# Kernel tuning notes

Hardware: AMD Instinct MI355X
Metric: run time of the kernel (lower is better)

The kernel has to match this reference:

```python
import jax, jax.numpy as jnp
import numpy as np
import math

HIDDEN = 1024
Q_SIZE = 1024
KV_SIZE = 1024
OUT_SIZE = 1024
N_HEADS = 16
D_K = HIDDEN // N_HEADS


def setup_inputs() -> dict:
    key = jax.random.key(0)
    ks = jax.random.split(key, 9)
    b, s, t = 8, 2048, 512
    sc = 0.02
    return {
        "hiddens": jax.random.normal(ks[0], (b, s, KV_SIZE), jnp.float32),
        "query_hiddens": jax.random.normal(ks[1], (b, t, Q_SIZE), jnp.float32),
        "mask": jax.random.randint(ks[2], (b, s), 0, 2, jnp.int32),
        "W_q": jax.random.normal(ks[3], (Q_SIZE, HIDDEN), jnp.float32) * sc,
        "b_q": jnp.zeros((HIDDEN,), jnp.float32),
        "W_k": jax.random.normal(ks[4], (KV_SIZE, HIDDEN), jnp.float32) * sc,
        "W_v": jax.random.normal(ks[5], (KV_SIZE, HIDDEN), jnp.float32) * sc,
        "W_o": jax.random.normal(ks[6], (HIDDEN, OUT_SIZE), jnp.float32) * sc,
        "b_o": jnp.zeros((OUT_SIZE,), jnp.float32),
    }


def reference(hiddens, query_hiddens, mask, W_q, b_q, W_k, W_v, W_o, b_o):
    b, t, _ = query_hiddens.shape
    s = hiddens.shape[1]
    # projections (dropout p=0 in eval -> identity)
    Q = (query_hiddens @ W_q + b_q).reshape(b, t, N_HEADS, D_K)
    K = (hiddens @ W_k).reshape(b, s, N_HEADS, D_K)
    V = (hiddens @ W_v).reshape(b, s, N_HEADS, D_K)
    # scores: [b, t, s, h] matching e = (Q*K).sum(-1)/sqrt(d_k)
    e = jnp.einsum('bthd,bshd->btsh', Q, K) / math.sqrt(D_K)
    neg = (1.0 - mask.astype(e.dtype)) * (-1e20)  # [b, s]
    e = e + neg[:, None, :, None]
    a = jax.nn.softmax(e, axis=2)  # softmax over seqlen
    concat = jnp.einsum('btsh,bshd->bthd', a, V).reshape(b, t, HIDDEN)
    context = concat @ W_o + b_o
    return context, a.mean(axis=-1)
```

## Files before the change

kernel.cpp:

```cpp
#include <hip/hip_runtime.h>
#include <hip/hip_bf16.h>

using short8 = __attribute__((ext_vector_type(8))) short;
using f32x4  = __attribute__((ext_vector_type(4))) float;

#define LSK 72

#define GLDS(gptr, lptr) __builtin_amdgcn_global_load_lds( \
    (const __attribute__((address_space(1))) void*)(gptr), \
    (__attribute__((address_space(3))) void*)(lptr), 16, 0, 0)

static __device__ __forceinline__ short f2b(float f) {
    unsigned u = __builtin_bit_cast(unsigned, f);
    unsigned r = (u + 0x7fffu + ((u >> 16) & 1u)) >> 16;
    return (short)r;
}

__global__ void cvt_bf16(const float* __restrict__ in, short* __restrict__ out, int n) {
    int i = (blockIdx.x * 256 + threadIdx.x) * 4;
    if (i >= n) return;
    float4 v = *(const float4*)(in + i);
    short4 o = make_short4(f2b(v.x), f2b(v.y), f2b(v.z), f2b(v.w));
    *(short4*)(out + i) = o;
}

__global__ void cvt_t_bf16(const float* __restrict__ W, short* __restrict__ Wt, int K, int N) {
    __shared__ short tile[32][33];
    int n0 = blockIdx.x * 32, k0 = blockIdx.y * 32;
    int tx = threadIdx.x, ty = threadIdx.y;
#pragma unroll
    for (int i = 0; i < 4; i++) {
        int r = ty + i * 8;
        tile[r][tx] = f2b(W[(size_t)(k0 + r) * N + n0 + tx]);
    }
    __syncthreads();
#pragma unroll
    for (int i = 0; i < 4; i++) {
        int r = ty + i * 8;
        Wt[(size_t)(n0 + r) * K + k0 + tx] = tile[tx][r];
    }
}

__global__ __launch_bounds__(256) void gemm128(
    const short* __restrict__ A, const short* __restrict__ Bt,
    const float* __restrict__ bias, void* __restrict__ Cout, void* __restrict__ Cout2,
    int M, int mode)
{
    __shared__ short As[128 * 64];
    __shared__ short Bs[128 * 64];
    const int tid = threadIdx.x;
    const int w = tid >> 6, L = tid & 63, quad = L >> 4, l16 = L & 15;

    const int lin = blockIdx.y * gridDim.x + blockIdx.x;
    const int xcd = lin & 7, idx = lin >> 3;
    const int mPer = gridDim.y >> 3;
    const int my = xcd * mPer + idx / gridDim.x;
    const int nx = idx % gridDim.x;
    const int n0 = nx * 128, m0 = my * 128;

    const int K = 1024;
    const int mrow0 = (w >> 1) * 64, ncol0 = (w & 1) * 64;

    const int srow_in = L >> 3;
    const int sgcol   = ((L & 7) ^ (srow_in & 7)) * 8;

    f32x4 acc[4][4];
#pragma unroll
    for (int mi = 0; mi < 4; mi++)
#pragma unroll
        for (int ni = 0; ni < 4; ni++) acc[mi][ni] = (f32x4){0.f, 0.f, 0.f, 0.f};

    for (int k0 = 0; k0 < K; k0 += 64) {
#pragma unroll
        for (int j = 0; j < 4; j++) {
            int c = w * 4 + j;
            int row = c * 8 + srow_in;
            const short* ga = A  + (size_t)(m0 + row) * K + k0 + sgcol;
            const short* gb = Bt + (size_t)(n0 + row) * K + k0 + sgcol;
            GLDS(ga, &As[c * 512]);
            GLDS(gb, &Bs[c * 512]);
        }
        __syncthreads();
#pragma unroll
        for (int kk = 0; kk < 64; kk += 32) {
            int swz = (((kk >> 3) + quad) ^ (l16 & 7)) << 3;
            short8 af[4], bf[4];
#pragma unroll
            for (int mi = 0; mi < 4; mi++)
                af[mi] = *(const short8*)&As[(mrow0 + mi * 16 + l16) * 64 + swz];
#pragma unroll
            for (int ni = 0; ni < 4; ni++)
                bf[ni] = *(const short8*)&Bs[(ncol0 + ni * 16 + l16) * 64 + swz];
#pragma unroll
            for (int mi = 0; mi < 4; mi++)
#pragma unroll
                for (int ni = 0; ni < 4; ni++)
                    acc[mi][ni] = __builtin_amdgcn_mfma_f32_16x16x32_bf16(af[mi], bf[ni], acc[mi][ni], 0, 0, 0);
        }
        __syncthreads();
    }
#pragma unroll
    for (int ni = 0; ni < 4; ni++) {
        int n = n0 + ncol0 + ni * 16 + l16;
        float bv = (mode != 2 && bias) ? bias[n] : 0.f;
#pragma unroll
        for (int mi = 0; mi < 4; mi++) {
#pragma unroll
            for (int r = 0; r < 4; r++) {
                int m = m0 + mrow0 + mi * 16 + quad * 4 + r;
                float v = acc[mi][ni][r] + bv;
                if (mode == 1)      ((float*)Cout)[(size_t)m * 1024 + n] = v;
                else if (mode == 0) ((short*)Cout)[(size_t)m * 1024 + n] = f2b(v);
                else {
                    if (n < 1024) ((short*)Cout)[(size_t)m * 1024 + n] = f2b(v);
                    else {
                        int h = (n - 1024) >> 6, d = n & 63;
                        int b = m >> 11, s = m & 2047;
                        ((short*)Cout2)[(((size_t)b * 16 + h) * 64 + d) * 2048 + s] = f2b(v);
                    }
                }
            }
        }
    }
}

__global__ __launch_bounds__(512) void attn_flash(
    const short* __restrict__ Qb, const short* __restrict__ Kb, const short* __restrict__ Vtb,
    const int* __restrict__ mask, short* __restrict__ Cb, float* __restrict__ lse)
{
    __shared__ short Qs[128 * 64];
    __shared__ short Ks[128 * 64];
    __shared__ short Vts[128 * 64];
    __shared__ short Ps[128 * LSK];
    __shared__ float neg[128];
    const int tid = threadIdx.x;
    const int w = tid >> 6, L = tid & 63, quad = L >> 4, l16 = L & 15;
    const int t0 = blockIdx.x * 128, h = blockIdx.y, b = blockIdx.z;
    const int S = 2048, T = 512, H = 1024;
    const int trow = w * 16;
    const int srow = L >> 3;
    const int sg   = ((L & 7) ^ srow) * 8;

#pragma unroll
    for (int j = 0; j < 2; j++) {
        int row = w * 16 + j * 8 + srow;
        GLDS(Qb + ((size_t)b * T + t0 + row) * H + h * 64 + sg, &Qs[(w * 16 + j * 8) * 64]);
    }
    __syncthreads();
    short8 aq[2];
#pragma unroll
    for (int kk = 0; kk < 2; kk++)
        aq[kk] = *(const short8*)&Qs[(trow + l16) * 64 + ((kk * 4 + quad) ^ (l16 & 7)) * 8];

    f32x4 Oacc[4];
#pragma unroll
    for (int nt = 0; nt < 4; nt++) Oacc[nt] = (f32x4){0.f, 0.f, 0.f, 0.f};
    float lsum[4] = {0.f, 0.f, 0.f, 0.f};

    for (int s0 = 0; s0 < S; s0 += 128) {
#pragma unroll
        for (int j = 0; j < 2; j++) {
            int krow = w * 16 + j * 8 + srow;
            GLDS(Kb + ((size_t)b * S + s0 + krow) * H + h * 64 + sg, &Ks[(w * 16 + j * 8) * 64]);
            int c = w * 2 + j, hf = c >> 3, d0 = (c & 7) * 8;
            GLDS(Vtb + (((size_t)b * 16 + h) * 64 + d0 + srow) * S + s0 + hf * 64 + sg, &Vts[c * 512]);
        }
        if (tid < 128) neg[tid] = mask[(size_t)b * S + s0 + tid] ? 0.f : -1e20f;
        __syncthreads();
#pragma unroll
        for (int hf = 0; hf < 2; hf++) {
            f32x4 sacc[4];
#pragma unroll
            for (int nt = 0; nt < 4; nt++) sacc[nt] = (f32x4){0.f, 0.f, 0.f, 0.f};
#pragma unroll
            for (int kk = 0; kk < 2; kk++) {
#pragma unroll
                for (int nt = 0; nt < 4; nt++) {
                    short8 bf = *(const short8*)&Ks[(hf * 64 + nt * 16 + l16) * 64 + ((kk * 4 + quad) ^ (l16 & 7)) * 8];
                    sacc[nt] = __builtin_amdgcn_mfma_f32_16x16x32_bf16(aq[kk], bf, sacc[nt], 0, 0, 0);
                }
            }
#pragma unroll
            for (int nt = 0; nt < 4; nt++) {
                float ng = neg[hf * 64 + nt * 16 + l16];
#pragma unroll
                for (int r = 0; r < 4; r++) {
                    float e = __expf(fmaf(sacc[nt][r], 0.125f, ng));
                    lsum[r] += e;
                    Ps[(trow + quad * 4 + r) * LSK + nt * 16 + l16] = f2b(e);
                }
            }
#pragma unroll
            for (int kk = 0; kk < 2; kk++) {
                short8 af = *(const short8*)&Ps[(trow + l16) * LSK + kk * 32 + quad * 8];
#pragma unroll
                for (int nt = 0; nt < 4; nt++) {
                    short8 bf = *(const short8*)&Vts[hf * 4096 + (nt * 16 + l16) * 64 + ((kk * 4 + quad) ^ (l16 & 7)) * 8];
                    Oacc[nt] = __builtin_amdgcn_mfma_f32_16x16x32_bf16(af, bf, Oacc[nt], 0, 0, 0);
                }
            }
        }
        __syncthreads();
    }
#pragma unroll
    for (int r = 0; r < 4; r++) {
#pragma unroll
        for (int off = 1; off < 16; off <<= 1)
            lsum[r] += __shfl_xor(lsum[r], off, 64);
    }
#pragma unroll
    for (int r = 0; r < 4; r++) {
        float inv = 1.0f / lsum[r];
        int t = t0 + trow + quad * 4 + r;
#pragma unroll
        for (int nt = 0; nt < 4; nt++) {
            int d = nt * 16 + l16;
            Cb[((size_t)b * T + t) * H + h * 64 + d] = f2b(Oacc[nt][r] * inv);
        }
        if (l16 == 0)
            lse[((size_t)b * 16 + h) * T + t] = __logf(lsum[r]);
    }
}

__global__ __launch_bounds__(256) void attn_amean(
    const short* __restrict__ Qb, const short* __restrict__ Kb,
    const int* __restrict__ mask, const float* __restrict__ lse, float* __restrict__ outA)
{
    __shared__ short Qs[64 * 64];
    __shared__ short Ks[64 * 64];
    __shared__ float neg[64];
    __shared__ float lss[16 * 64];
    const int tid = threadIdx.x;
    const int w = tid >> 6, L = tid & 63, quad = L >> 4, l16 = L & 15;
    const int s0 = blockIdx.x * 64, t0 = blockIdx.y * 64, b = blockIdx.z;
    const int S = 2048, T = 512, H = 1024;
    const int srow = L >> 3;
    const int sg   = ((L & 7) ^ srow) * 8;

    if (tid < 64) neg[tid] = mask[(size_t)b * S + s0 + tid] ? 0.f : -1e20f;
    for (int i = tid; i < 16 * 64; i += 256) {
        int hh = i >> 6, tt = i & 63;
        lss[i] = lse[((size_t)b * 16 + hh) * T + t0 + tt];
    }
    float am[4][4] = {};
    for (int h = 0; h < 16; h++) {
        __syncthreads();
#pragma unroll
        for (int j = 0; j < 2; j++) {
            int row = w * 16 + j * 8 + srow;
            GLDS(Qb + ((size_t)b * T + t0 + row) * H + h * 64 + sg, &Qs[(w * 16 + j * 8) * 64]);
            GLDS(Kb + ((size_t)b * S + s0 + row) * H + h * 64 + sg, &Ks[(w * 16 + j * 8) * 64]);
        }
        __syncthreads();
        short8 aq[2];
#pragma unroll
        for (int kk = 0; kk < 2; kk++)
            aq[kk] = *(const short8*)&Qs[(w * 16 + l16) * 64 + ((kk * 4 + quad) ^ (l16 & 7)) * 8];
        f32x4 sacc[4];
#pragma unroll
        for (int nt = 0; nt < 4; nt++) sacc[nt] = (f32x4){0.f, 0.f, 0.f, 0.f};
#pragma unroll
        for (int kk = 0; kk < 2; kk++) {
#pragma unroll
            for (int nt = 0; nt < 4; nt++) {
                short8 bf = *(const short8*)&Ks[(nt * 16 + l16) * 64 + ((kk * 4 + quad) ^ (l16 & 7)) * 8];
                sacc[nt] = __builtin_amdgcn_mfma_f32_16x16x32_bf16(aq[kk], bf, sacc[nt], 0, 0, 0);
            }
        }
#pragma unroll
        for (int nt = 0; nt < 4; nt++) {
            float ng = neg[nt * 16 + l16];
#pragma unroll
            for (int r = 0; r < 4; r++) {
                int trow = w * 16 + quad * 4 + r;
                am[nt][r] += __expf(fmaf(sacc[nt][r], 0.125f, ng - lss[h * 64 + trow]));
            }
        }
    }
#pragma unroll
    for (int r = 0; r < 4; r++) {
        int t = t0 + w * 16 + quad * 4 + r;
#pragma unroll
        for (int nt = 0; nt < 4; nt++) {
            int s = s0 + nt * 16 + l16;
            outA[((size_t)b * T + t) * S + s] = am[nt][r] * 0.0625f;
        }
    }
}

extern "C" void kernel_launch(void* const* d_in, const int* in_sizes, int n_in,
                              void* d_out, int out_size, void* d_ws, size_t ws_size,
                              hipStream_t stream) {
    const float* hiddens = (const float*)d_in[0];
    const float* query   = (const float*)d_in[1];
    const int*   mask    = (const int*)d_in[2];
    const float* W_q = (const float*)d_in[3];
    const float* b_q = (const float*)d_in[4];
    const float* W_k = (const float*)d_in[5];
    const float* W_v = (const float*)d_in[6];
    const float* W_o = (const float*)d_in[7];
    const float* b_o = (const float*)d_in[8];
    float* out = (float*)d_out;

    constexpr size_t N_H  = 8UL * 2048 * 1024;
    constexpr size_t N_QH = 8UL * 512 * 1024;
    constexpr size_t N_W  = 1024UL * 1024;
    char* ws = (char*)d_ws;
    short* Hb   = (short*)(ws);
    short* QHb  = (short*)(ws + N_H * 2);
    short* Wqt  = (short*)(ws + N_H * 2 + N_QH * 2);
    short* Wkt  = Wqt + N_W;
    short* Wvt  = Wkt + N_W;
    short* Wot  = Wvt + N_W;
    short* Qb   = Wot + N_W;
    short* Kb   = Qb + N_QH;
    short* Vtb  = Kb + N_H;
    short* Cb   = Vtb + N_H;
    float* lseP = (float*)(Cb + N_QH);

    cvt_bf16<<<16384, 256, 0, stream>>>(hiddens, Hb, (int)N_H);
    cvt_bf16<<<4096, 256, 0, stream>>>(query, QHb, (int)N_QH);
    dim3 tgrid(32, 32), tblk(32, 8);
    cvt_t_bf16<<<tgrid, tblk, 0, stream>>>(W_q, Wqt, 1024, 1024);
    cvt_t_bf16<<<tgrid, tblk, 0, stream>>>(W_k, Wkt, 1024, 1024);
    cvt_t_bf16<<<tgrid, tblk, 0, stream>>>(W_v, Wvt, 1024, 1024);
    cvt_t_bf16<<<tgrid, tblk, 0, stream>>>(W_o, Wot, 1024, 1024);

    gemm128<<<dim3(8, 32), 256, 0, stream>>>(QHb, Wqt, b_q, Qb, nullptr, 4096, 0);
    gemm128<<<dim3(16, 128), 256, 0, stream>>>(Hb, Wkt, nullptr, Kb, Vtb, 16384, 2);

    attn_flash<<<dim3(4, 16, 8), 512, 0, stream>>>(Qb, Kb, Vtb, mask, Cb, lseP);

    gemm128<<<dim3(8, 32), 256, 0, stream>>>(Cb, Wot, b_o, out, nullptr, 4096, 1);
    attn_amean<<<dim3(32, 8, 8), 256, 0, stream>>>(Qb, Kb, mask, lseP, out + N_QH);
}
```

Baseline: 433.8 us.

## Shrink GEMM tile to 128x64 and merge weight transpose launches

The GEMM tile moves from 128x128 to 128x64. Each wave now computes 32x64 and the loads are split across waves as 16 A chunks and 8 B chunks, which doubles the grid for the Q, KV and output projections and adds a launch_bounds occupancy hint. The aim is better CU occupancy and load balance on the small 4096-row GEMMs, paid for with lower data reuse per tile and more global traffic for the A operand. The four weight transpose-convert kernels are also merged into one launch using blockIdx.z.

```diff
diff --git a/kernel.cpp b/kernel.cpp
--- a/kernel.cpp
+++ b/kernel.cpp
@@ -24,8 +24,14 @@
     *(short4*)(out + i) = o;
 }
 
-__global__ void cvt_t_bf16(const float* __restrict__ W, short* __restrict__ Wt, int K, int N) {
+__global__ void cvt_t4(const float* __restrict__ W0, const float* __restrict__ W1,
+                       const float* __restrict__ W2, const float* __restrict__ W3,
+                       short* __restrict__ Wt0) {
     __shared__ short tile[32][33];
+    const float* Ws[4] = {W0, W1, W2, W3};
+    const float* W = Ws[blockIdx.z];
+    short* Wt = Wt0 + (size_t)blockIdx.z * 1024 * 1024;
+    const int K = 1024, N = 1024;
     int n0 = blockIdx.x * 32, k0 = blockIdx.y * 32;
     int tx = threadIdx.x, ty = threadIdx.y;
 #pragma unroll
@@ -41,13 +47,13 @@
     }
 }
 
-__global__ __launch_bounds__(256) void gemm128(
+__global__ __launch_bounds__(256, 4) void gemm128(
     const short* __restrict__ A, const short* __restrict__ Bt,
     const float* __restrict__ bias, void* __restrict__ Cout, void* __restrict__ Cout2,
     int M, int mode)
 {
     __shared__ short As[128 * 64];
-    __shared__ short Bs[128 * 64];
+    __shared__ short Bs[64 * 64];
     const int tid = threadIdx.x;
     const int w = tid >> 6, L = tid & 63, quad = L >> 4, l16 = L & 15;
 
@@ -56,43 +62,44 @@
     const int mPer = gridDim.y >> 3;
     const int my = xcd * mPer + idx / gridDim.x;
     const int nx = idx % gridDim.x;
-    const int n0 = nx * 128, m0 = my * 128;
+    const int n0 = nx * 64, m0 = my * 128;
 
     const int K = 1024;
-    const int mrow0 = (w >> 1) * 64, ncol0 = (w & 1) * 64;
-
+    const int mrow0 = w * 32;
     const int srow_in = L >> 3;
     const int sgcol   = ((L & 7) ^ (srow_in & 7)) * 8;
 
-    f32x4 acc[4][4];
-#pragma unroll
-    for (int mi = 0; mi < 4; mi++)
+    f32x4 acc[2][4];
+#pragma unroll
+    for (int mi = 0; mi < 2; mi++)
 #pragma unroll
         for (int ni = 0; ni < 4; ni++) acc[mi][ni] = (f32x4){0.f, 0.f, 0.f, 0.f};
 
     for (int k0 = 0; k0 < K; k0 += 64) {
 #pragma unroll
-        for (int j = 0; j < 4; j++) {
-            int c = w * 4 + j;
-            int row = c * 8 + srow_in;
-            const short* ga = A  + (size_t)(m0 + row) * K + k0 + sgcol;
-            const short* gb = Bt + (size_t)(n0 + row) * K + k0 + sgcol;
-            GLDS(ga, &As[c * 512]);
-            GLDS(gb, &Bs[c * 512]);
+        for (int j = 0; j < 6; j++) {
+            int c = w * 6 + j;
+            if (c < 16) {
+                int row = c * 8 + srow_in;
+                GLDS(A + (size_t)(m0 + row) * K + k0 + sgcol, &As[c * 512]);
+            } else {
+                int row = (c - 16) * 8 + srow_in;
+                GLDS(Bt + (size_t)(n0 + row) * K + k0 + sgcol, &Bs[(c - 16) * 512]);
+            }
         }
         __syncthreads();
 #pragma unroll
         for (int kk = 0; kk < 64; kk += 32) {
             int swz = (((kk >> 3) + quad) ^ (l16 & 7)) << 3;
-            short8 af[4], bf[4];
-#pragma unroll
-            for (int mi = 0; mi < 4; mi++)
+            short8 af[2], bf[4];
+#pragma unroll
+            for (int mi = 0; mi < 2; mi++)
                 af[mi] = *(const short8*)&As[(mrow0 + mi * 16 + l16) * 64 + swz];
 #pragma unroll
             for (int ni = 0; ni < 4; ni++)
-                bf[ni] = *(const short8*)&Bs[(ncol0 + ni * 16 + l16) * 64 + swz];
-#pragma unroll
-            for (int mi = 0; mi < 4; mi++)
+                bf[ni] = *(const short8*)&Bs[(ni * 16 + l16) * 64 + swz];
+#pragma unroll
+            for (int mi = 0; mi < 2; mi++)
 #pragma unroll
                 for (int ni = 0; ni < 4; ni++)
                     acc[mi][ni] = __builtin_amdgcn_mfma_f32_16x16x32_bf16(af[mi], bf[ni], acc[mi][ni], 0, 0, 0);
@@ -101,10 +108,10 @@
     }
 #pragma unroll
     for (int ni = 0; ni < 4; ni++) {
-        int n = n0 + ncol0 + ni * 16 + l16;
+        int n = n0 + ni * 16 + l16;
         float bv = (mode != 2 && bias) ? bias[n] : 0.f;
 #pragma unroll
-        for (int mi = 0; mi < 4; mi++) {
+        for (int mi = 0; mi < 2; mi++) {
 #pragma unroll
             for (int r = 0; r < 4; r++) {
                 int m = m0 + mrow0 + mi * 16 + quad * 4 + r;
@@ -320,17 +327,13 @@
 
     cvt_bf16<<<16384, 256, 0, stream>>>(hiddens, Hb, (int)N_H);
     cvt_bf16<<<4096, 256, 0, stream>>>(query, QHb, (int)N_QH);
-    dim3 tgrid(32, 32), tblk(32, 8);
-    cvt_t_bf16<<<tgrid, tblk, 0, stream>>>(W_q, Wqt, 1024, 1024);
-    cvt_t_bf16<<<tgrid, tblk, 0, stream>>>(W_k, Wkt, 1024, 1024);
-    cvt_t_bf16<<<tgrid, tblk, 0, stream>>>(W_v, Wvt, 1024, 1024);
-    cvt_t_bf16<<<tgrid, tblk, 0, stream>>>(W_o, Wot, 1024, 1024);
-
-    gemm128<<<dim3(8, 32), 256, 0, stream>>>(QHb, Wqt, b_q, Qb, nullptr, 4096, 0);
-    gemm128<<<dim3(16, 128), 256, 0, stream>>>(Hb, Wkt, nullptr, Kb, Vtb, 16384, 2);
+    cvt_t4<<<dim3(32, 32, 4), dim3(32, 8), 0, stream>>>(W_q, W_k, W_v, W_o, Wqt);
+
+    gemm128<<<dim3(16, 32), 256, 0, stream>>>(QHb, Wqt, b_q, Qb, nullptr, 4096, 0);
+    gemm128<<<dim3(32, 128), 256, 0, stream>>>(Hb, Wkt, nullptr, Kb, Vtb, 16384, 2);
 
     attn_flash<<<dim3(4, 16, 8), 512, 0, stream>>>(Qb, Kb, Vtb, mask, Cb, lseP);
 
-    gemm128<<<dim3(8, 32), 256, 0, stream>>>(Cb, Wot, b_o, out, nullptr, 4096, 1);
+    gemm128<<<dim3(16, 32), 256, 0, stream>>>(Cb, Wot, b_o, out, nullptr, 4096, 1);
     attn_amean<<<dim3(32, 8, 8), 256, 0, stream>>>(Qb, Kb, mask, lseP, out + N_QH);
 }
```

New measurement: 414.5 us. 4.5% less time.
